# Kernel tuning notes

Measured on AMD Instinct MI355X. Metric: run time of the kernel, lower is better.

The kernel has to match this reference:

```python
import jax, jax.numpy as jnp
import numpy as np

B, S, D = 2, 2048, 2048
H, HKV, DH = 16, 4, 128   # query heads, kv heads, head dim
N_REP = H // HKV
ROPE_BASE = 10000.0


def rotate_half(x):
    x1, x2 = x[..., : DH // 2], x[..., DH // 2 :]
    return jnp.concatenate((-x2, x1), axis=-1)


def rope_tables(seq_len, dtype=jnp.float32):
    inv_freq = 1.0 / (ROPE_BASE ** (jnp.arange(0, DH, 2, dtype=jnp.float32) / DH))
    t = jnp.arange(seq_len, dtype=jnp.float32)
    freqs = jnp.outer(t, inv_freq)                 # [S, DH/2]
    emb = jnp.concatenate((freqs, freqs), axis=-1)  # [S, DH]
    return jnp.cos(emb).astype(dtype), jnp.sin(emb).astype(dtype)


def setup_inputs() -> dict:
    key = jax.random.key(0)
    k1, k2, k3, k4, k5 = jax.random.split(key, 5)
    scale = 1.0 / np.sqrt(D)
    return {
        "hidden_states": jax.random.normal(k1, (B, S, D), dtype=jnp.float32),
        "position_ids": jnp.tile(jnp.arange(S, dtype=jnp.int32)[None, :], (B, 1)),
        "wq": jax.random.normal(k2, (D, H * DH), dtype=jnp.float32) * scale,
        "wk": jax.random.normal(k3, (D, HKV * DH), dtype=jnp.float32) * scale,
        "wv": jax.random.normal(k4, (D, HKV * DH), dtype=jnp.float32) * scale,
        "wo": jax.random.normal(k5, (H * DH, D), dtype=jnp.float32) * scale,
    }


def reference(hidden_states, position_ids, wq, wk, wv, wo):
    x = hidden_states
    b, s, _ = x.shape

    # QKV projections -> [B, H(kv), S, DH]
    q = (x @ wq).reshape(b, s, H, DH).transpose(0, 2, 1, 3)
    k = (x @ wk).reshape(b, s, HKV, DH).transpose(0, 2, 1, 3)
    v = (x @ wv).reshape(b, s, HKV, DH).transpose(0, 2, 1, 3)

    # Rotary position embedding
    cos_t, sin_t = rope_tables(s, x.dtype)
    cos = cos_t[position_ids][:, None, :, :]  # [B,1,S,DH]
    sin = sin_t[position_ids][:, None, :, :]
    q = q * cos + rotate_half(q) * sin
    k = k * cos + rotate_half(k) * sin

    # GQA: repeat KV heads to match query heads
    k = jnp.repeat(k, N_REP, axis=1)  # [B,H,S,DH]
    v = jnp.repeat(v, N_REP, axis=1)

    # Causal SDPA
    scores = jnp.einsum("bhqd,bhkd->bhqk", q, k) / jnp.sqrt(
        jnp.asarray(DH, x.dtype)
    )
    causal = jnp.tril(jnp.ones((s, s), dtype=bool))
    scores = jnp.where(causal[None, None], scores, jnp.asarray(-1e9, x.dtype))
    attn = jax.nn.softmax(scores, axis=-1)
    out = jnp.einsum("bhqk,bhkd->bhqd", attn, v)  # [B,H,S,DH]

    out = out.transpose(0, 2, 1, 3).reshape(b, s, H * DH)
    return out @ wo
```

## Files before the change

### kernel.cpp

```cpp
#include <hip/hip_runtime.h>
#include <cmath>

typedef unsigned short u16;
typedef float floatx4 __attribute__((ext_vector_type(4)));
typedef short short8 __attribute__((ext_vector_type(8)));
typedef short short4v __attribute__((ext_vector_type(4)));
typedef __bf16 bf16x8 __attribute__((ext_vector_type(8)));

#define GLOBAL_AS __attribute__((address_space(1)))
#define LDS_AS __attribute__((address_space(3)))

#define S_LEN 2048
#define D_MODEL 2048
#define NH 16
#define NKV 4
#define DHEAD 128
#define SM_SCALE 0.08838834764831843f
#define K2 (SM_SCALE * 1.4426950408889634f)

__device__ __forceinline__ u16 f2bf(float f) {
    unsigned int u = __builtin_bit_cast(unsigned int, f);
    u += 0x7fffu + ((u >> 16) & 1u);
    return (u16)(u >> 16);
}
__device__ __forceinline__ u16 f2bfr(float f) {
    unsigned int u = __builtin_bit_cast(unsigned int, f);
    return (u16)((u + 0x8000u) >> 16);
}
__device__ __forceinline__ float bf2f(u16 x) {
    unsigned int u = ((unsigned int)x) << 16;
    return __builtin_bit_cast(float, u);
}
__device__ __forceinline__ floatx4 zf4() {
    floatx4 z; z[0] = 0.f; z[1] = 0.f; z[2] = 0.f; z[3] = 0.f; return z;
}
__device__ __forceinline__ floatx4 mfma16(short8 a, short8 b, floatx4 c) {
    return __builtin_amdgcn_mfma_f32_16x16x32_bf16(
        __builtin_bit_cast(bf16x8, a), __builtin_bit_cast(bf16x8, b), c, 0, 0, 0);
}
__device__ __forceinline__ floatx4 mfma16k16(short4v a, short4v b, floatx4 c) {
    return __builtin_amdgcn_mfma_f32_16x16x16bf16_1k(a, b, c, 0, 0, 0);
}
__device__ __forceinline__ void async16(const u16* g, u16* l) {
    __builtin_amdgcn_global_load_lds((GLOBAL_AS void*)g, (LDS_AS void*)l, 16, 0, 0);
}

__global__ void cast_x_kernel(const float4* __restrict__ in, ushort4* __restrict__ out) {
    int i = blockIdx.x * 256 + threadIdx.x;
    float4 v = in[i];
    ushort4 o;
    o.x = f2bf(v.x); o.y = f2bf(v.y); o.z = f2bf(v.z); o.w = f2bf(v.w);
    out[i] = o;
}

__global__ void transpose_cast_kernel(const float* __restrict__ in, u16* __restrict__ out,
                                      int R, int C) {
    __shared__ float tile[32][33];
    int tx = threadIdx.x & 31, ty = threadIdx.x >> 5;
    int bx = blockIdx.x * 32;
    int by = blockIdx.y * 32;
#pragma unroll
    for (int i = 0; i < 32; i += 8)
        tile[ty + i][tx] = in[(size_t)(by + ty + i) * C + bx + tx];
    __syncthreads();
#pragma unroll
    for (int i = 0; i < 32; i += 8)
        out[(size_t)(bx + ty + i) * R + by + tx] = f2bf(tile[tx][ty + i]);
}

__global__ void rope_tables_kernel(float* __restrict__ cs_tab, float* __restrict__ sn_tab) {
    int idx = blockIdx.x * 256 + threadIdx.x;
    int p = idx >> 6, j = idx & 63;
    double e = (double)(2 * j) / 128.0;
    double invf = pow(10000.0, -e);
    float arg = (float)p * (float)invf;
    cs_tab[idx] = (float)cos((double)arg);
    sn_tab[idx] = (float)sin((double)arg);
}

__global__ void rope_apply_kernel(u16* __restrict__ Qb, u16* __restrict__ Kb,
                                  const int* __restrict__ pos,
                                  const float4* __restrict__ cs_tab,
                                  const float4* __restrict__ sn_tab) {
    int idx = blockIdx.x * 256 + threadIdx.x;
    int j4 = idx & 15;
    int s = (idx >> 4) & 2047;
    int r = idx >> 15;
    int hh = r % 20, b = r / 20;
    int p = pos[b * S_LEN + s];
    float4 cs = cs_tab[p * 16 + j4];
    float4 sn = sn_tab[p * 16 + j4];
    u16* base;
    if (hh < 16) base = Qb + (((size_t)(b * NH + hh)) * S_LEN + s) * DHEAD;
    else         base = Kb + (((size_t)(b * NKV + (hh - 16))) * S_LEN + s) * DHEAD;
    base += j4 * 4;
    ushort4 a = *(const ushort4*)(base);
    ushort4 c = *(const ushort4*)(base + 64);
    ushort4 oa, oc;
    float x1, x2;
    x1 = bf2f(a.x); x2 = bf2f(c.x); oa.x = f2bf(x1 * cs.x - x2 * sn.x); oc.x = f2bf(x2 * cs.x + x1 * sn.x);
    x1 = bf2f(a.y); x2 = bf2f(c.y); oa.y = f2bf(x1 * cs.y - x2 * sn.y); oc.y = f2bf(x2 * cs.y + x1 * sn.y);
    x1 = bf2f(a.z); x2 = bf2f(c.z); oa.z = f2bf(x1 * cs.z - x2 * sn.z); oc.z = f2bf(x2 * cs.z + x1 * sn.z);
    x1 = bf2f(a.w); x2 = bf2f(c.w); oa.w = f2bf(x1 * cs.w - x2 * sn.w); oc.w = f2bf(x2 * cs.w + x1 * sn.w);
    *(ushort4*)(base) = oa;
    *(ushort4*)(base + 64) = oc;
}

__device__ __forceinline__ void gemm_mainloop(const u16* __restrict__ A,
                                              const u16* __restrict__ Bt,
                                              int K, u16* ldsA, u16* ldsB,
                                              floatx4 acc[4][4]) {
    const int t = threadIdx.x;
    const int lane = t & 63, wave = t >> 6;
    const int wr = wave >> 1, wc = wave & 1;
    const int lr = lane & 15, q = lane >> 4;
    const int m0 = blockIdx.y * 128, n0 = blockIdx.x * 128;
    const int swz = lr & 7;

#pragma unroll
    for (int r = 0; r < 4; ++r)
#pragma unroll
        for (int c = 0; c < 4; ++c) acc[r][c] = zf4();

    for (int k0 = 0; k0 < K; k0 += 64) {
#pragma unroll
        for (int i = 0; i < 4; ++i) {
            int ci = i * 256 + t;
            int row = ci >> 3;
            int kc = ((ci & 7) ^ (row & 7)) << 3;
            async16(A + (size_t)(m0 + row) * K + k0 + kc, ldsA + (i * 256 + wave * 64) * 8);
            async16(Bt + (size_t)(n0 + row) * K + k0 + kc, ldsB + (i * 256 + wave * 64) * 8);
        }
        __syncthreads();
#pragma unroll
        for (int ks = 0; ks < 2; ++ks) {
            short8 af[4], bfr[4];
#pragma unroll
            for (int r = 0; r < 4; ++r)
                af[r] = *(const short8*)(ldsA + (wr * 64 + r * 16 + lr) * 64 +
                                         (((ks * 4 + q) ^ swz) << 3));
#pragma unroll
            for (int c = 0; c < 4; ++c)
                bfr[c] = *(const short8*)(ldsB + (wc * 64 + c * 16 + lr) * 64 +
                                          (((ks * 4 + q) ^ swz) << 3));
#pragma unroll
            for (int r = 0; r < 4; ++r)
#pragma unroll
                for (int c = 0; c < 4; ++c)
                    acc[r][c] = mfma16(af[r], bfr[c], acc[r][c]);
        }
        __syncthreads();
    }
}

__global__ void qkv_gemm_kernel(const u16* __restrict__ A, const u16* __restrict__ Bt,
                                u16* __restrict__ Qb, u16* __restrict__ Kb,
                                u16* __restrict__ Vt) {
    __shared__ u16 ldsA[128 * 64];
    __shared__ u16 ldsB[128 * 64];
    floatx4 acc[4][4];
    gemm_mainloop(A, Bt, D_MODEL, ldsA, ldsB, acc);

    const int t = threadIdx.x, lane = t & 63, wave = t >> 6;
    const int wr = wave >> 1, wc = wave & 1, lr = lane & 15, q = lane >> 4;
    const int m0 = blockIdx.y * 128 + wr * 64, n0 = blockIdx.x * 128 + wc * 64;
#pragma unroll
    for (int r = 0; r < 4; ++r)
#pragma unroll
        for (int c = 0; c < 4; ++c) {
            int gc = n0 + c * 16 + lr;
#pragma unroll
            for (int rr = 0; rr < 4; ++rr) {
                int grow = m0 + r * 16 + q * 4 + rr;
                int bb = grow >> 11, s = grow & 2047;
                u16 bv = f2bf(acc[r][c][rr]);
                int d = gc & 127;
                if (gc < 2048) {
                    int hh = gc >> 7;
                    Qb[(((size_t)(bb * NH + hh)) * S_LEN + s) * DHEAD + d] = bv;
                } else if (gc < 2560) {
                    int hh = (gc - 2048) >> 7;
                    Kb[(((size_t)(bb * NKV + hh)) * S_LEN + s) * DHEAD + d] = bv;
                } else {
                    int hh = (gc - 2560) >> 7;
                    int s2 = s ^ ((d & 8) >> 1);
                    Vt[(((size_t)(bb * NKV + hh)) * DHEAD + d) * S_LEN + s2] = bv;
                }
            }
        }
}

__global__ void out_gemm_kernel(const u16* __restrict__ A, const u16* __restrict__ Bt,
                                float* __restrict__ out) {
    __shared__ u16 ldsA[128 * 64];
    __shared__ u16 ldsB[128 * 64];
    floatx4 acc[4][4];
    gemm_mainloop(A, Bt, D_MODEL, ldsA, ldsB, acc);

    const int t = threadIdx.x, lane = t & 63, wave = t >> 6;
    const int wr = wave >> 1, wc = wave & 1, lr = lane & 15, q = lane >> 4;
    const int m0 = blockIdx.y * 128 + wr * 64, n0 = blockIdx.x * 128 + wc * 64;
#pragma unroll
    for (int r = 0; r < 4; ++r)
#pragma unroll
        for (int c = 0; c < 4; ++c) {
            int gc = n0 + c * 16 + lr;
#pragma unroll
            for (int rr = 0; rr < 4; ++rr) {
                int grow = m0 + r * 16 + q * 4 + rr;
                out[(size_t)grow * D_MODEL + gc] = acc[r][c][rr];
            }
        }
}

__global__ __launch_bounds__(256, 4) void fa_kernel(const u16* __restrict__ Qb,
                                                    const u16* __restrict__ Kb,
                                                    const u16* __restrict__ Vt,
                                                    u16* __restrict__ Ob) {
    __shared__ u16 ldsK[64 * 128];
    __shared__ u16 ldsV[128 * 64];

    const int t = threadIdx.x, lane = t & 63, wave = t >> 6;
    const int lr = lane & 15, q = lane >> 4;
    const int swz = lr & 7;

    const int bid = blockIdx.x;
    const int r4 = bid >> 8, j = bid & 255;
    const int p = j >> 3, lo = j & 7;
    const int bh = r4 * 8 + lo;
    int qt;
    if (r4 == 0) qt = p;
    else if (r4 == 1) qt = 31 - p;
    else if (r4 == 2) qt = p ^ 16;
    else qt = 31 - (p ^ 16);
    const int b = bh >> 4, h = bh & 15;
    const int kvh = h >> 2;

    const u16* Kp = Kb + (size_t)(b * NKV + kvh) * S_LEN * DHEAD;
    const u16* Vp = Vt + (size_t)(b * NKV + kvh) * DHEAD * S_LEN;
    const u16* Qp = Qb + ((size_t)((b * NH + h) * S_LEN) + qt * 64 + wave * 16) * DHEAD;

    short8 qf[4];
#pragma unroll
    for (int kk = 0; kk < 4; ++kk)
        qf[kk] = *(const short8*)(Qp + (size_t)lr * DHEAD + kk * 32 + q * 8);

    floatx4 accO[8];
#pragma unroll
    for (int d = 0; d < 8; ++d) accO[d] = zf4();
    float m_i = -3e38f, l_i = 0.f;

    const int nkt = qt + 1;
    for (int kt = 0; kt < nkt; ++kt) {
#pragma unroll
        for (int i = 0; i < 4; ++i) {
            int ci = i * 256 + t;
            int krow = ci >> 4, kc = ((ci & 15) ^ ((ci >> 4) & 7)) << 3;
            async16(Kp + (size_t)(kt * 64 + krow) * DHEAD + kc,
                    ldsK + (i * 256 + wave * 64) * 8);
            int dh = ci >> 3, vc = ((ci & 7) ^ ((ci >> 3) & 7)) << 3;
            async16(Vp + (size_t)dh * S_LEN + kt * 64 + vc,
                    ldsV + (i * 256 + wave * 64) * 8);
        }
        __syncthreads();

        floatx4 sc[4];
#pragma unroll
        for (int c = 0; c < 4; ++c) {
            sc[c] = zf4();
#pragma unroll
            for (int kk = 0; kk < 4; ++kk) {
                short8 kfr = *(const short8*)(ldsK + (c * 16 + lr) * DHEAD +
                                              (((kk * 4 + q) ^ swz) << 3));
                sc[c] = mfma16(kfr, qf[kk], sc[c]);
            }
        }

        if (kt == qt) {
            const int qrow = wave * 16 + lr;
#pragma unroll
            for (int c = 0; c < 4; ++c)
#pragma unroll
                for (int rr = 0; rr < 4; ++rr)
                    if (c * 16 + q * 4 + rr > qrow) sc[c][rr] = -3e38f;
        }

        float mx = -3e38f;
#pragma unroll
        for (int c = 0; c < 4; ++c)
#pragma unroll
            for (int rr = 0; rr < 4; ++rr) mx = fmaxf(mx, sc[c][rr]);
        mx = fmaxf(mx, __shfl_xor(mx, 16));
        mx = fmaxf(mx, __shfl_xor(mx, 32));
        float mnew = fmaxf(m_i, mx);
        float mk = mnew * K2;
        bool anyup = __any(mnew > m_i);
        float rs = 0.f;
#pragma unroll
        for (int c = 0; c < 4; ++c)
#pragma unroll
            for (int rr = 0; rr < 4; ++rr) {
                float pe = __builtin_amdgcn_exp2f(fmaf(sc[c][rr], K2, -mk));
                sc[c][rr] = pe;
                rs += pe;
            }
        rs += __shfl_xor(rs, 16);
        rs += __shfl_xor(rs, 32);
        if (anyup) {
            float alpha = __builtin_amdgcn_exp2f(fmaf(m_i, K2, -mk));
            l_i = l_i * alpha + rs;
#pragma unroll
            for (int d = 0; d < 8; ++d) accO[d] *= alpha;
        } else {
            l_i += rs;
        }
        m_i = mnew;

        short4v pb[4];
#pragma unroll
        for (int c = 0; c < 4; ++c) {
            pb[c][0] = (short)f2bfr(sc[c][0]);
            pb[c][1] = (short)f2bfr(sc[c][1]);
            pb[c][2] = (short)f2bfr(sc[c][2]);
            pb[c][3] = (short)f2bfr(sc[c][3]);
        }

#pragma unroll
        for (int ks = 0; ks < 4; ++ks)
#pragma unroll
            for (int d = 0; d < 8; ++d) {
                short4v vf = *(const short4v*)(ldsV + (d * 16 + lr) * 64 +
                                               (((ks * 2 + (q >> 1)) ^ swz) << 3) +
                                               (((q ^ (lr >> 3)) & 1) << 2));
                accO[d] = mfma16k16(vf, pb[ks], accO[d]);
            }
        __syncthreads();
    }

    const int tok = qt * 64 + wave * 16 + lr;
    const float inv = 1.0f / l_i;
    u16* orow = Ob + ((size_t)(b * S_LEN + tok)) * (NH * DHEAD) + h * DHEAD + q * 4;
#pragma unroll
    for (int d = 0; d < 8; ++d) {
        ushort4 o;
        o.x = f2bf(accO[d][0] * inv);
        o.y = f2bf(accO[d][1] * inv);
        o.z = f2bf(accO[d][2] * inv);
        o.w = f2bf(accO[d][3] * inv);
        *(ushort4*)(orow + d * 16) = o;
    }
}

extern "C" void kernel_launch(void* const* d_in, const int* in_sizes, int n_in,
                              void* d_out, int out_size, void* d_ws, size_t ws_size,
                              hipStream_t stream) {
    const float* X  = (const float*)d_in[0];
    const int* pos  = (const int*)d_in[1];
    const float* wq = (const float*)d_in[2];
    const float* wk = (const float*)d_in[3];
    const float* wv = (const float*)d_in[4];
    const float* wo = (const float*)d_in[5];
    float* out = (float*)d_out;

    char* w = (char*)d_ws;
    u16* Xbf    = (u16*)(w);
    u16* Wqkv   = (u16*)(w + 16777216);
    u16* Wo     = (u16*)(w + 29360128);
    u16* Qb     = (u16*)(w + 37748736);
    u16* Kb     = (u16*)(w + 54525952);
    u16* Vt     = (u16*)(w + 58720256);
    u16* Ob     = (u16*)(w + 62914560);
    float* cst  = (float*)(w + 79691776);
    float* snt  = (float*)(w + 80216064);

    cast_x_kernel<<<8192, 256, 0, stream>>>((const float4*)X, (ushort4*)Xbf);
    transpose_cast_kernel<<<dim3(64, 64), 256, 0, stream>>>(wq, Wqkv, 2048, 2048);
    transpose_cast_kernel<<<dim3(16, 64), 256, 0, stream>>>(wk, Wqkv + (size_t)2048 * 2048, 2048, 512);
    transpose_cast_kernel<<<dim3(16, 64), 256, 0, stream>>>(wv, Wqkv + (size_t)2560 * 2048, 2048, 512);
    transpose_cast_kernel<<<dim3(64, 64), 256, 0, stream>>>(wo, Wo, 2048, 2048);
    rope_tables_kernel<<<512, 256, 0, stream>>>(cst, snt);
    qkv_gemm_kernel<<<dim3(24, 32), 256, 0, stream>>>(Xbf, Wqkv, Qb, Kb, Vt);
    rope_apply_kernel<<<5120, 256, 0, stream>>>(Qb, Kb, pos, (const float4*)cst, (const float4*)snt);
    fa_kernel<<<1024, 256, 0, stream>>>(Qb, Kb, Vt, Ob);
    out_gemm_kernel<<<dim3(16, 32), 256, 0, stream>>>(Ob, Wo, out);
}
```

Baseline: 312.7 us.

## Make attention kernel persistent with atomic work queue, longest tiles first

Replaces the static block-to-tile mapping in the flash-attention kernel with a persistent grid of 768 blocks. Each block pulls (query tile, batch-head) items from a global atomic counter, ordered from the longest causal tiles down to the shortest. The counter is reset inside the RoPE kernel, which runs earlier on the same stream. The aim is better load balance across CUs for the triangular causal workload, at the cost of one atomic and one barrier per item and a fixed residency assumption.

```diff
diff --git a/kernel.cpp b/kernel.cpp
--- a/kernel.cpp
+++ b/kernel.cpp
@@ -81,8 +81,10 @@
 __global__ void rope_apply_kernel(u16* __restrict__ Qb, u16* __restrict__ Kb,
                                   const int* __restrict__ pos,
                                   const float4* __restrict__ cs_tab,
-                                  const float4* __restrict__ sn_tab) {
+                                  const float4* __restrict__ sn_tab,
+                                  int* __restrict__ qcount) {
     int idx = blockIdx.x * 256 + threadIdx.x;
+    if (idx == 0) *qcount = 0;
     int j4 = idx & 15;
     int s = (idx >> 4) & 2047;
     int r = idx >> 15;
@@ -216,138 +218,139 @@
 __global__ __launch_bounds__(256, 4) void fa_kernel(const u16* __restrict__ Qb,
                                                     const u16* __restrict__ Kb,
                                                     const u16* __restrict__ Vt,
-                                                    u16* __restrict__ Ob) {
+                                                    u16* __restrict__ Ob,
+                                                    int* __restrict__ qcount) {
     __shared__ u16 ldsK[64 * 128];
     __shared__ u16 ldsV[128 * 64];
+    __shared__ int item_s;
 
     const int t = threadIdx.x, lane = t & 63, wave = t >> 6;
     const int lr = lane & 15, q = lane >> 4;
     const int swz = lr & 7;
 
-    const int bid = blockIdx.x;
-    const int r4 = bid >> 8, j = bid & 255;
-    const int p = j >> 3, lo = j & 7;
-    const int bh = r4 * 8 + lo;
-    int qt;
-    if (r4 == 0) qt = p;
-    else if (r4 == 1) qt = 31 - p;
-    else if (r4 == 2) qt = p ^ 16;
-    else qt = 31 - (p ^ 16);
-    const int b = bh >> 4, h = bh & 15;
-    const int kvh = h >> 2;
-
-    const u16* Kp = Kb + (size_t)(b * NKV + kvh) * S_LEN * DHEAD;
-    const u16* Vp = Vt + (size_t)(b * NKV + kvh) * DHEAD * S_LEN;
-    const u16* Qp = Qb + ((size_t)((b * NH + h) * S_LEN) + qt * 64 + wave * 16) * DHEAD;
-
-    short8 qf[4];
-#pragma unroll
-    for (int kk = 0; kk < 4; ++kk)
-        qf[kk] = *(const short8*)(Qp + (size_t)lr * DHEAD + kk * 32 + q * 8);
-
-    floatx4 accO[8];
-#pragma unroll
-    for (int d = 0; d < 8; ++d) accO[d] = zf4();
-    float m_i = -3e38f, l_i = 0.f;
-
-    const int nkt = qt + 1;
-    for (int kt = 0; kt < nkt; ++kt) {
-#pragma unroll
-        for (int i = 0; i < 4; ++i) {
-            int ci = i * 256 + t;
-            int krow = ci >> 4, kc = ((ci & 15) ^ ((ci >> 4) & 7)) << 3;
-            async16(Kp + (size_t)(kt * 64 + krow) * DHEAD + kc,
-                    ldsK + (i * 256 + wave * 64) * 8);
-            int dh = ci >> 3, vc = ((ci & 7) ^ ((ci >> 3) & 7)) << 3;
-            async16(Vp + (size_t)dh * S_LEN + kt * 64 + vc,
-                    ldsV + (i * 256 + wave * 64) * 8);
-        }
+    for (;;) {
+        if (t == 0) item_s = atomicAdd(qcount, 1);
         __syncthreads();
-
-        floatx4 sc[4];
-#pragma unroll
-        for (int c = 0; c < 4; ++c) {
-            sc[c] = zf4();
-#pragma unroll
-            for (int kk = 0; kk < 4; ++kk) {
-                short8 kfr = *(const short8*)(ldsK + (c * 16 + lr) * DHEAD +
-                                              (((kk * 4 + q) ^ swz) << 3));
-                sc[c] = mfma16(kfr, qf[kk], sc[c]);
-            }
-        }
-
-        if (kt == qt) {
-            const int qrow = wave * 16 + lr;
+        const int item = item_s;
+        if (item >= 1024) break;
+        const int qt = 31 - (item >> 5);
+        const int bh = item & 31;
+        const int b = bh >> 4, h = bh & 15;
+        const int kvh = h >> 2;
+
+        const u16* Kp = Kb + (size_t)(b * NKV + kvh) * S_LEN * DHEAD;
+        const u16* Vp = Vt + (size_t)(b * NKV + kvh) * DHEAD * S_LEN;
+        const u16* Qp = Qb + ((size_t)((b * NH + h) * S_LEN) + qt * 64 + wave * 16) * DHEAD;
+
+        short8 qf[4];
+#pragma unroll
+        for (int kk = 0; kk < 4; ++kk)
+            qf[kk] = *(const short8*)(Qp + (size_t)lr * DHEAD + kk * 32 + q * 8);
+
+        floatx4 accO[8];
+#pragma unroll
+        for (int d = 0; d < 8; ++d) accO[d] = zf4();
+        float m_i = -3e38f, l_i = 0.f;
+
+        const int nkt = qt + 1;
+        for (int kt = 0; kt < nkt; ++kt) {
+#pragma unroll
+            for (int i = 0; i < 4; ++i) {
+                int ci = i * 256 + t;
+                int krow = ci >> 4, kc = ((ci & 15) ^ ((ci >> 4) & 7)) << 3;
+                async16(Kp + (size_t)(kt * 64 + krow) * DHEAD + kc,
+                        ldsK + (i * 256 + wave * 64) * 8);
+                int dh = ci >> 3, vc = ((ci & 7) ^ ((ci >> 3) & 7)) << 3;
+                async16(Vp + (size_t)dh * S_LEN + kt * 64 + vc,
+                        ldsV + (i * 256 + wave * 64) * 8);
+            }
+            __syncthreads();
+
+            floatx4 sc[4];
+#pragma unroll
+            for (int c = 0; c < 4; ++c) {
+                sc[c] = zf4();
+#pragma unroll
+                for (int kk = 0; kk < 4; ++kk) {
+                    short8 kfr = *(const short8*)(ldsK + (c * 16 + lr) * DHEAD +
+                                                  (((kk * 4 + q) ^ swz) << 3));
+                    sc[c] = mfma16(kfr, qf[kk], sc[c]);
+                }
+            }
+
+            if (kt == qt) {
+                const int qrow = wave * 16 + lr;
+#pragma unroll
+                for (int c = 0; c < 4; ++c)
+#pragma unroll
+                    for (int rr = 0; rr < 4; ++rr)
+                        if (c * 16 + q * 4 + rr > qrow) sc[c][rr] = -3e38f;
+            }
+
+            float mx = -3e38f;
 #pragma unroll
             for (int c = 0; c < 4; ++c)
 #pragma unroll
-                for (int rr = 0; rr < 4; ++rr)
-                    if (c * 16 + q * 4 + rr > qrow) sc[c][rr] = -3e38f;
-        }
-
-        float mx = -3e38f;
-#pragma unroll
-        for (int c = 0; c < 4; ++c)
-#pragma unroll
-            for (int rr = 0; rr < 4; ++rr) mx = fmaxf(mx, sc[c][rr]);
-        mx = fmaxf(mx, __shfl_xor(mx, 16));
-        mx = fmaxf(mx, __shfl_xor(mx, 32));
-        float mnew = fmaxf(m_i, mx);
-        float mk = mnew * K2;
-        bool anyup = __any(mnew > m_i);
-        float rs = 0.f;
-#pragma unroll
-        for (int c = 0; c < 4; ++c)
-#pragma unroll
-            for (int rr = 0; rr < 4; ++rr) {
-                float pe = __builtin_amdgcn_exp2f(fmaf(sc[c][rr], K2, -mk));
-                sc[c][rr] = pe;
-                rs += pe;
-            }
-        rs += __shfl_xor(rs, 16);
-        rs += __shfl_xor(rs, 32);
-        if (anyup) {
-            float alpha = __builtin_amdgcn_exp2f(fmaf(m_i, K2, -mk));
-            l_i = l_i * alpha + rs;
-#pragma unroll
-            for (int d = 0; d < 8; ++d) accO[d] *= alpha;
-        } else {
-            l_i += rs;
-        }
-        m_i = mnew;
-
-        short4v pb[4];
-#pragma unroll
-        for (int c = 0; c < 4; ++c) {
-            pb[c][0] = (short)f2bfr(sc[c][0]);
-            pb[c][1] = (short)f2bfr(sc[c][1]);
-            pb[c][2] = (short)f2bfr(sc[c][2]);
-            pb[c][3] = (short)f2bfr(sc[c][3]);
-        }
-
-#pragma unroll
-        for (int ks = 0; ks < 4; ++ks)
-#pragma unroll
-            for (int d = 0; d < 8; ++d) {
-                short4v vf = *(const short4v*)(ldsV + (d * 16 + lr) * 64 +
-                                               (((ks * 2 + (q >> 1)) ^ swz) << 3) +
-                                               (((q ^ (lr >> 3)) & 1) << 2));
-                accO[d] = mfma16k16(vf, pb[ks], accO[d]);
-            }
-        __syncthreads();
-    }
-
-    const int tok = qt * 64 + wave * 16 + lr;
-    const float inv = 1.0f / l_i;
-    u16* orow = Ob + ((size_t)(b * S_LEN + tok)) * (NH * DHEAD) + h * DHEAD + q * 4;
-#pragma unroll
-    for (int d = 0; d < 8; ++d) {
-        ushort4 o;
-        o.x = f2bf(accO[d][0] * inv);
-        o.y = f2bf(accO[d][1] * inv);
-        o.z = f2bf(accO[d][2] * inv);
-        o.w = f2bf(accO[d][3] * inv);
-        *(ushort4*)(orow + d * 16) = o;
+                for (int rr = 0; rr < 4; ++rr) mx = fmaxf(mx, sc[c][rr]);
+            mx = fmaxf(mx, __shfl_xor(mx, 16));
+            mx = fmaxf(mx, __shfl_xor(mx, 32));
+            float mnew = fmaxf(m_i, mx);
+            float mk = mnew * K2;
+            bool anyup = __any(mnew > m_i);
+            float rs = 0.f;
+#pragma unroll
+            for (int c = 0; c < 4; ++c)
+#pragma unroll
+                for (int rr = 0; rr < 4; ++rr) {
+                    float pe = __builtin_amdgcn_exp2f(fmaf(sc[c][rr], K2, -mk));
+                    sc[c][rr] = pe;
+                    rs += pe;
+                }
+            rs += __shfl_xor(rs, 16);
+            rs += __shfl_xor(rs, 32);
+            if (anyup) {
+                float alpha = __builtin_amdgcn_exp2f(fmaf(m_i, K2, -mk));
+                l_i = l_i * alpha + rs;
+#pragma unroll
+                for (int d = 0; d < 8; ++d) accO[d] *= alpha;
+            } else {
+                l_i += rs;
+            }
+            m_i = mnew;
+
+            short4v pb[4];
+#pragma unroll
+            for (int c = 0; c < 4; ++c) {
+                pb[c][0] = (short)f2bfr(sc[c][0]);
+                pb[c][1] = (short)f2bfr(sc[c][1]);
+                pb[c][2] = (short)f2bfr(sc[c][2]);
+                pb[c][3] = (short)f2bfr(sc[c][3]);
+            }
+
+#pragma unroll
+            for (int ks = 0; ks < 4; ++ks)
+#pragma unroll
+                for (int d = 0; d < 8; ++d) {
+                    short4v vf = *(const short4v*)(ldsV + (d * 16 + lr) * 64 +
+                                                   (((ks * 2 + (q >> 1)) ^ swz) << 3) +
+                                                   (((q ^ (lr >> 3)) & 1) << 2));
+                    accO[d] = mfma16k16(vf, pb[ks], accO[d]);
+                }
+            __syncthreads();
+        }
+
+        const int tok = qt * 64 + wave * 16 + lr;
+        const float inv = 1.0f / l_i;
+        u16* orow = Ob + ((size_t)(b * S_LEN + tok)) * (NH * DHEAD) + h * DHEAD + q * 4;
+#pragma unroll
+        for (int d = 0; d < 8; ++d) {
+            ushort4 o;
+            o.x = f2bf(accO[d][0] * inv);
+            o.y = f2bf(accO[d][1] * inv);
+            o.z = f2bf(accO[d][2] * inv);
+            o.w = f2bf(accO[d][3] * inv);
+            *(ushort4*)(orow + d * 16) = o;
+        }
     }
 }
 
@@ -372,6 +375,7 @@
     u16* Ob     = (u16*)(w + 62914560);
     float* cst  = (float*)(w + 79691776);
     float* snt  = (float*)(w + 80216064);
+    int* qcount = (int*)(w + 80740352);
 
     cast_x_kernel<<<8192, 256, 0, stream>>>((const float4*)X, (ushort4*)Xbf);
     transpose_cast_kernel<<<dim3(64, 64), 256, 0, stream>>>(wq, Wqkv, 2048, 2048);
@@ -380,7 +384,7 @@
     transpose_cast_kernel<<<dim3(64, 64), 256, 0, stream>>>(wo, Wo, 2048, 2048);
     rope_tables_kernel<<<512, 256, 0, stream>>>(cst, snt);
     qkv_gemm_kernel<<<dim3(24, 32), 256, 0, stream>>>(Xbf, Wqkv, Qb, Kb, Vt);
-    rope_apply_kernel<<<5120, 256, 0, stream>>>(Qb, Kb, pos, (const float4*)cst, (const float4*)snt);
-    fa_kernel<<<1024, 256, 0, stream>>>(Qb, Kb, Vt, Ob);
+    rope_apply_kernel<<<5120, 256, 0, stream>>>(Qb, Kb, pos, (const float4*)cst, (const float4*)snt, qcount);
+    fa_kernel<<<768, 256, 0, stream>>>(Qb, Kb, Vt, Ob, qcount);
     out_gemm_kernel<<<dim3(16, 32), 256, 0, stream>>>(Ob, Wo, out);
 }
```

After: 316.2 us. Within noise of the previous version (+1.1%).
